# Kernel optimization log

Hardware: AMD Instinct MI355X
Metric: run time of the kernel (lower is better)

The kernel has to match this reference:

```python
import jax, jax.numpy as jnp
import numpy as np

B, L, D, H, S, V, K = 2, 64, 1024, 512, 50000, 40000, 32
SLM_LOGITS_SCALE = 0.1
BN_EPS = 1e-5


def setup_inputs() -> dict:
    key = jax.random.key(0)
    ks = jax.random.split(key, 8)
    return {
        "cached_embeddings": jax.random.normal(ks[0], (B, L, D), dtype=jnp.float32),
        "bn_gamma": jnp.ones((L,), jnp.float32),
        "bn_beta": jnp.zeros((L,), jnp.float32),
        "W1": jax.random.normal(ks[1], (D, H), dtype=jnp.float32) * 0.02,
        "b1": jnp.zeros((H,), jnp.float32),
        "W2": jax.random.normal(ks[2], (H, S), dtype=jnp.float32) * 0.02,
        "b2": jnp.zeros((S,), jnp.float32),
        "W_slm": jax.random.normal(ks[3], (H, V), dtype=jnp.float32) * 0.02,
        "b_slm": jnp.zeros((V,), jnp.float32),
        # fixed degree k=32 with values 1/min(deg,k) = 1/32 (full-degree rows)
        "sl_weights": jnp.full((S, K), 1.0 / K, jnp.float32),
        "sl_idx": jax.random.randint(ks[4], (S, K), 0, V, dtype=jnp.int32),
    }


def reference(cached_embeddings, bn_gamma, bn_beta, W1, b1, W2, b2,
              W_slm, b_slm, sl_weights, sl_idx):
    x = cached_embeddings  # [B, L, D]
    # BatchNorm1d(win_size): channels are sequence positions; stats over (B, D)
    mean = jnp.mean(x, axis=(0, 2), keepdims=True)
    var = jnp.var(x, axis=(0, 2), keepdims=True)
    xn = (x - mean) * jax.lax.rsqrt(var + BN_EPS)
    x = xn * bn_gamma[None, :, None] + bn_beta[None, :, None]
    # DenseEncoder: hidden + sense logits
    h = jax.nn.relu(jnp.einsum('bld,dh->blh', x, W1) + b1)  # [B, L, H]
    y = jnp.einsum('blh,hs->bls', h, W2) + b2                # [B, L, S]
    # SLM head: lemma logits
    v = jnp.einsum('blh,hv->blv', h, W_slm) + b_slm          # [B, L, V]
    # sparse sense->lemma matmul == weighted bounded-degree gather-sum
    g = v[..., sl_idx]                                       # [B, L, S, K]
    slm_logits = jnp.einsum('blsk,sk->bls', g, sl_weights)   # [B, L, S]
    return y + slm_logits * SLM_LOGITS_SCALE
```

## Files before the change

### kernel.cpp

```cpp
#include <hip/hip_runtime.h>

#define LL 64
#define DD 1024
#define HH 512
#define SS 50000
#define VV 40000
#define KD 32
#define MM 128

typedef __bf16 bf16_t;
typedef __bf16 bf16x8 __attribute__((ext_vector_type(8)));
typedef __bf16 bf16x4 __attribute__((ext_vector_type(4)));
typedef __bf16 bf16x2 __attribute__((ext_vector_type(2)));
typedef float f32x4 __attribute__((ext_vector_type(4)));

__device__ __forceinline__ void async_ld16(const void* g, void* l) {
    __builtin_amdgcn_global_load_lds(
        (const __attribute__((address_space(1))) void*)g,
        (__attribute__((address_space(3))) void*)l, 16, 0, 0);
}

__global__ __launch_bounds__(256) void k_bn(const float* __restrict__ x,
        const float* __restrict__ gamma, const float* __restrict__ beta,
        bf16_t* __restrict__ xn) {
    int l = blockIdx.x;
    int t = threadIdx.x;
    int b = t >> 7;
    int d0 = (t & 127) << 3;
    const float* xp = x + (size_t)(b * LL + l) * DD + d0;
    float4 v0 = *(const float4*)xp;
    float4 v1 = *(const float4*)(xp + 4);
    float s  = v0.x + v0.y + v0.z + v0.w + v1.x + v1.y + v1.z + v1.w;
    float ss = v0.x*v0.x + v0.y*v0.y + v0.z*v0.z + v0.w*v0.w
             + v1.x*v1.x + v1.y*v1.y + v1.z*v1.z + v1.w*v1.w;
    #pragma unroll
    for (int off = 32; off > 0; off >>= 1) {
        s  += __shfl_xor(s, off);
        ss += __shfl_xor(ss, off);
    }
    __shared__ float red[8];
    int wv = t >> 6, ln = t & 63;
    if (ln == 0) { red[wv] = s; red[4 + wv] = ss; }
    __syncthreads();
    float tot  = red[0] + red[1] + red[2] + red[3];
    float tots = red[4] + red[5] + red[6] + red[7];
    float mean = tot * (1.0f / 2048.0f);
    float var  = tots * (1.0f / 2048.0f) - mean * mean;
    float rstd = rsqrtf(var + 1e-5f);
    float g   = gamma[l] * rstd;
    float ofs = beta[l] - mean * g;
    bf16x8 o;
    o[0] = (bf16_t)(v0.x * g + ofs);
    o[1] = (bf16_t)(v0.y * g + ofs);
    o[2] = (bf16_t)(v0.z * g + ofs);
    o[3] = (bf16_t)(v0.w * g + ofs);
    o[4] = (bf16_t)(v1.x * g + ofs);
    o[5] = (bf16_t)(v1.y * g + ofs);
    o[6] = (bf16_t)(v1.z * g + ofs);
    o[7] = (bf16_t)(v1.w * g + ofs);
    *(bf16x8*)(xn + (size_t)(b * LL + l) * DD + d0) = o;
}

__global__ __launch_bounds__(256) void k_gemm1(const bf16_t* __restrict__ xn,
        const float* __restrict__ W1, const float* __restrict__ b1,
        bf16_t* __restrict__ h) {
    int t = threadIdx.x;
    int wv = t >> 6, lane = t & 63;
    int c = lane & 15, q = lane >> 4;
    int tile = blockIdx.x * 4 + wv;
    int tm = tile >> 5, tn = tile & 31;
    int col = tn * 16 + c;
    f32x4 acc = {};
    for (int kk = 0; kk < DD; kk += 32) {
        bf16x8 afr = *(const bf16x8*)(xn + (size_t)(tm * 16 + c) * DD + kk + q * 8);
        bf16x8 bfr;
        #pragma unroll
        for (int j = 0; j < 8; ++j)
            bfr[j] = (bf16_t)W1[(size_t)(kk + q * 8 + j) * HH + col];
        acc = __builtin_amdgcn_mfma_f32_16x16x32_bf16(afr, bfr, acc, 0, 0, 0);
    }
    float bias = b1[col];
    #pragma unroll
    for (int r = 0; r < 4; ++r) {
        int m = tm * 16 + q * 4 + r;
        float v = acc[r] + bias;
        h[(size_t)m * HH + col] = (bf16_t)(v > 0.f ? v : 0.f);
    }
}

__global__ __launch_bounds__(256) void k_gemm_v(const bf16_t* __restrict__ h,
        const float* __restrict__ Wslm, const float* __restrict__ bslm,
        bf16_t* __restrict__ vT) {
    __shared__ float wt[2][32 * 64];
    int t = threadIdx.x;
    int wv = t >> 6, lane = t & 63;
    int c = lane & 15, q = lane >> 4;
    int nb = blockIdx.x * 64;
    int col = nb + wv * 16 + c;
    int r  = t >> 4, sg = t & 15;
    const float* g0 = Wslm + (size_t)r        * VV + nb + sg * 4;
    const float* g1 = Wslm + (size_t)(r + 16) * VV + nb + sg * 4;

    #define STAGE_V(buf, kk) do { \
        async_ld16(g0 + (size_t)(kk) * VV, &wt[buf][t * 4]); \
        async_ld16(g1 + (size_t)(kk) * VV, &wt[buf][(t + 256) * 4]); } while (0)

    STAGE_V(0, 0);
    f32x4 acc[8] = {};
    #pragma unroll 1
    for (int step = 0; step < 16; ++step) {
        int cur = step & 1;
        __syncthreads();
        if (step < 15) STAGE_V(cur ^ 1, (step + 1) * 32);
        int kk = step * 32;
        bf16x8 bfr;
        #pragma unroll
        for (int j = 0; j < 8; ++j)
            bfr[j] = (bf16_t)wt[cur][(q * 8 + j) * 64 + wv * 16 + c];
        #pragma unroll
        for (int ms = 0; ms < 8; ++ms) {
            bf16x8 afr = *(const bf16x8*)(h + (size_t)(ms * 16 + c) * HH + kk + q * 8);
            acc[ms] = __builtin_amdgcn_mfma_f32_16x16x32_bf16(afr, bfr, acc[ms], 0, 0, 0);
        }
    }
    float bias = bslm[col];
    #pragma unroll
    for (int ms = 0; ms < 8; ++ms) {
        bf16x4 o;
        #pragma unroll
        for (int rr = 0; rr < 4; ++rr) o[rr] = (bf16_t)(acc[ms][rr] + bias);
        *(bf16x4*)(vT + (size_t)col * MM + ms * 16 + q * 4) = o;
    }
    #undef STAGE_V
}

__global__ __launch_bounds__(256) void k_gather(const bf16_t* __restrict__ vT,
        const float* __restrict__ slw, const int* __restrict__ slidx,
        bf16_t* __restrict__ slm) {
    int t = threadIdx.x;
    int wv = t >> 6, lane = t & 63;
    int s = blockIdx.x * 4 + wv;
    int idv = slidx[(size_t)s * KD + (lane & 31)];
    float wgt = slw[(size_t)s * KD + (lane & 31)];
    unsigned int u[KD];
    #pragma unroll
    for (int k = 0; k < KD; ++k) {
        int id = __shfl(idv, k);
        u[k] = *(const unsigned int*)(vT + (size_t)id * MM + lane * 2);
    }
    float a0 = 0.f, a1 = 0.f;
    #pragma unroll
    for (int k = 0; k < KD; ++k) {
        float w = __shfl(wgt, k);
        a0 += w * __uint_as_float(u[k] << 16);
        a1 += w * __uint_as_float(u[k] & 0xffff0000u);
    }
    bf16x2 o;
    o[0] = (bf16_t)a0;
    o[1] = (bf16_t)a1;
    *(bf16x2*)(slm + (size_t)s * MM + lane * 2) = o;
}

__global__ __launch_bounds__(256) void k_gemm_y(const bf16_t* __restrict__ h,
        const float* __restrict__ W2, const float* __restrict__ b2,
        const bf16_t* __restrict__ slm, float* __restrict__ out) {
    __shared__ float wt[2][32 * 64];
    int t = threadIdx.x;
    int wv = t >> 6, lane = t & 63;
    int c = lane & 15, q = lane >> 4;
    int nb = blockIdx.x * 64;
    int col = nb + wv * 16 + c;
    int r  = t >> 4, sg = t & 15;
    int sgc = nb + sg * 4;
    bool ok = (sgc + 4 <= SS);
    const float* g0 = ok ? (W2 + (size_t)r        * SS + sgc) : W2;
    const float* g1 = ok ? (W2 + (size_t)(r + 16) * SS + sgc) : W2;

    #define STAGE_Y(buf, kk) do { \
        async_ld16(g0 + (size_t)(kk) * SS, &wt[buf][t * 4]); \
        async_ld16(g1 + (size_t)(kk) * SS, &wt[buf][(t + 256) * 4]); } while (0)

    STAGE_Y(0, 0);
    f32x4 acc[8] = {};
    #pragma unroll 1
    for (int step = 0; step < 16; ++step) {
        int cur = step & 1;
        __syncthreads();
        if (step < 15) STAGE_Y(cur ^ 1, (step + 1) * 32);
        int kk = step * 32;
        bf16x8 bfr;
        #pragma unroll
        for (int j = 0; j < 8; ++j)
            bfr[j] = (bf16_t)wt[cur][(q * 8 + j) * 64 + wv * 16 + c];
        #pragma unroll
        for (int ms = 0; ms < 8; ++ms) {
            bf16x8 afr = *(const bf16x8*)(h + (size_t)(ms * 16 + c) * HH + kk + q * 8);
            acc[ms] = __builtin_amdgcn_mfma_f32_16x16x32_bf16(afr, bfr, acc[ms], 0, 0, 0);
        }
    }
    if (col < SS) {
        float bias = b2[col];
        #pragma unroll
        for (int ms = 0; ms < 8; ++ms) {
            bf16x4 sv = *(const bf16x4*)(slm + (size_t)col * MM + ms * 16 + q * 4);
            #pragma unroll
            for (int rr = 0; rr < 4; ++rr) {
                int m = ms * 16 + q * 4 + rr;
                out[(size_t)m * SS + col] = acc[ms][rr] + bias + 0.1f * (float)sv[rr];
            }
        }
    }
    #undef STAGE_Y
}

extern "C" void kernel_launch(void* const* d_in, const int* in_sizes, int n_in,
                              void* d_out, int out_size, void* d_ws, size_t ws_size,
                              hipStream_t stream) {
    const float* x     = (const float*)d_in[0];
    const float* gamma = (const float*)d_in[1];
    const float* beta  = (const float*)d_in[2];
    const float* W1    = (const float*)d_in[3];
    const float* b1    = (const float*)d_in[4];
    const float* W2    = (const float*)d_in[5];
    const float* b2    = (const float*)d_in[6];
    const float* Wslm  = (const float*)d_in[7];
    const float* bslm  = (const float*)d_in[8];
    const float* slw   = (const float*)d_in[9];
    const int*   slidx = (const int*)d_in[10];
    float* out = (float*)d_out;

    char* ws = (char*)d_ws;
    bf16_t* xn  = (bf16_t*)ws;
    bf16_t* h   = (bf16_t*)(ws + 262144);
    bf16_t* vT  = (bf16_t*)(ws + 393216);
    bf16_t* slm = (bf16_t*)(ws + 10633216);

    k_bn    <<<64,    256, 0, stream>>>(x, gamma, beta, xn);
    k_gemm1 <<<64,    256, 0, stream>>>(xn, W1, b1, h);
    k_gemm_v<<<625,   256, 0, stream>>>(h, Wslm, bslm, vT);
    k_gather<<<12500, 256, 0, stream>>>(vT, slw, slidx, slm);
    k_gemm_y<<<782,   256, 0, stream>>>(h, W2, b2, slm, out);
}
```

Before: 352.3 us.

## Store lemma logits as fp8, split-K gemm1, deeper staging with staggered K order

The lemma-logit intermediate vT is now stored as fp8 e4m3 instead of bf16, which halves the write traffic in k_gemm_v and the random-gather traffic in k_gather, at the cost of precision in the sense-lemma term. k_gemm1 now splits K across two waves per 16x16 tile and combines the partial sums through shared memory, giving 256 blocks instead of 64. The W_slm and W2 GEMMs stage 64 K-rows per step instead of 32, using 8 steps and twice the LDS. They also rotate each block's starting K offset by a per-block phase, likely to spread concurrent loads across memory channels.

```diff
diff --git a/kernel.cpp b/kernel.cpp
--- a/kernel.cpp
+++ b/kernel.cpp
@@ -1,4 +1,5 @@
 #include <hip/hip_runtime.h>
+#include <hip/hip_fp8.h>
 
 #define LL 64
 #define DD 1024
@@ -61,17 +62,17 @@
     *(bf16x8*)(xn + (size_t)(b * LL + l) * DD + d0) = o;
 }
 
-__global__ __launch_bounds__(256) void k_gemm1(const bf16_t* __restrict__ xn,
+__global__ __launch_bounds__(128) void k_gemm1(const bf16_t* __restrict__ xn,
         const float* __restrict__ W1, const float* __restrict__ b1,
         bf16_t* __restrict__ h) {
     int t = threadIdx.x;
     int wv = t >> 6, lane = t & 63;
     int c = lane & 15, q = lane >> 4;
-    int tile = blockIdx.x * 4 + wv;
+    int tile = blockIdx.x;
     int tm = tile >> 5, tn = tile & 31;
     int col = tn * 16 + c;
     f32x4 acc = {};
-    for (int kk = 0; kk < DD; kk += 32) {
+    for (int kk = wv * 512; kk < wv * 512 + 512; kk += 32) {
         bf16x8 afr = *(const bf16x8*)(xn + (size_t)(tm * 16 + c) * DD + kk + q * 8);
         bf16x8 bfr;
         #pragma unroll
@@ -79,62 +80,79 @@
             bfr[j] = (bf16_t)W1[(size_t)(kk + q * 8 + j) * HH + col];
         acc = __builtin_amdgcn_mfma_f32_16x16x32_bf16(afr, bfr, acc, 0, 0, 0);
     }
-    float bias = b1[col];
-    #pragma unroll
-    for (int r = 0; r < 4; ++r) {
-        int m = tm * 16 + q * 4 + r;
-        float v = acc[r] + bias;
-        h[(size_t)m * HH + col] = (bf16_t)(v > 0.f ? v : 0.f);
+    __shared__ float red[64 * 4];
+    if (wv == 1) {
+        #pragma unroll
+        for (int r = 0; r < 4; ++r) red[lane * 4 + r] = acc[r];
+    }
+    __syncthreads();
+    if (wv == 0) {
+        float bias = b1[col];
+        #pragma unroll
+        for (int r = 0; r < 4; ++r) {
+            int m = tm * 16 + q * 4 + r;
+            float v = acc[r] + red[lane * 4 + r] + bias;
+            h[(size_t)m * HH + col] = (bf16_t)(v > 0.f ? v : 0.f);
+        }
     }
 }
 
 __global__ __launch_bounds__(256) void k_gemm_v(const bf16_t* __restrict__ h,
         const float* __restrict__ Wslm, const float* __restrict__ bslm,
-        bf16_t* __restrict__ vT) {
-    __shared__ float wt[2][32 * 64];
+        unsigned char* __restrict__ vT8) {
+    __shared__ float wt[2][64 * 64];
     int t = threadIdx.x;
     int wv = t >> 6, lane = t & 63;
     int c = lane & 15, q = lane >> 4;
     int nb = blockIdx.x * 64;
     int col = nb + wv * 16 + c;
     int r  = t >> 4, sg = t & 15;
-    const float* g0 = Wslm + (size_t)r        * VV + nb + sg * 4;
-    const float* g1 = Wslm + (size_t)(r + 16) * VV + nb + sg * 4;
+    int phase = (blockIdx.x * 5) & 7;
+    const float* gbase = Wslm + (size_t)r * VV + nb + sg * 4;
 
     #define STAGE_V(buf, kk) do { \
-        async_ld16(g0 + (size_t)(kk) * VV, &wt[buf][t * 4]); \
-        async_ld16(g1 + (size_t)(kk) * VV, &wt[buf][(t + 256) * 4]); } while (0)
-
-    STAGE_V(0, 0);
+        _Pragma("unroll") \
+        for (int i = 0; i < 4; ++i) \
+            async_ld16(gbase + (size_t)((kk) + 16 * i) * VV, \
+                       &wt[buf][t * 4 + i * 1024]); } while (0)
+
+    STAGE_V(0, phase * 64);
     f32x4 acc[8] = {};
     #pragma unroll 1
-    for (int step = 0; step < 16; ++step) {
+    for (int step = 0; step < 8; ++step) {
         int cur = step & 1;
         __syncthreads();
-        if (step < 15) STAGE_V(cur ^ 1, (step + 1) * 32);
-        int kk = step * 32;
-        bf16x8 bfr;
-        #pragma unroll
-        for (int j = 0; j < 8; ++j)
-            bfr[j] = (bf16_t)wt[cur][(q * 8 + j) * 64 + wv * 16 + c];
-        #pragma unroll
-        for (int ms = 0; ms < 8; ++ms) {
-            bf16x8 afr = *(const bf16x8*)(h + (size_t)(ms * 16 + c) * HH + kk + q * 8);
-            acc[ms] = __builtin_amdgcn_mfma_f32_16x16x32_bf16(afr, bfr, acc[ms], 0, 0, 0);
+        if (step < 7) STAGE_V(cur ^ 1, (((step + 1 + phase) & 7) * 64));
+        int kk = ((step + phase) & 7) * 64;
+        #pragma unroll
+        for (int kh = 0; kh < 2; ++kh) {
+            bf16x8 bfr;
+            #pragma unroll
+            for (int j = 0; j < 8; ++j)
+                bfr[j] = (bf16_t)wt[cur][(kh * 32 + q * 8 + j) * 64 + wv * 16 + c];
+            #pragma unroll
+            for (int ms = 0; ms < 8; ++ms) {
+                bf16x8 afr = *(const bf16x8*)(h + (size_t)(ms * 16 + c) * HH
+                                              + kk + kh * 32 + q * 8);
+                acc[ms] = __builtin_amdgcn_mfma_f32_16x16x32_bf16(afr, bfr, acc[ms], 0, 0, 0);
+            }
         }
     }
     float bias = bslm[col];
     #pragma unroll
     for (int ms = 0; ms < 8; ++ms) {
-        bf16x4 o;
-        #pragma unroll
-        for (int rr = 0; rr < 4; ++rr) o[rr] = (bf16_t)(acc[ms][rr] + bias);
-        *(bf16x4*)(vT + (size_t)col * MM + ms * 16 + q * 4) = o;
+        union { unsigned int u; unsigned char b[4]; } pk;
+        #pragma unroll
+        for (int rr = 0; rr < 4; ++rr) {
+            __hip_fp8_e4m3 f8(acc[ms][rr] + bias);
+            pk.b[rr] = f8.__x;
+        }
+        *(unsigned int*)(vT8 + (size_t)col * MM + ms * 16 + q * 4) = pk.u;
     }
     #undef STAGE_V
 }
 
-__global__ __launch_bounds__(256) void k_gather(const bf16_t* __restrict__ vT,
+__global__ __launch_bounds__(256) void k_gather(const unsigned char* __restrict__ vT8,
         const float* __restrict__ slw, const int* __restrict__ slidx,
         bf16_t* __restrict__ slm) {
     int t = threadIdx.x;
@@ -142,18 +160,21 @@
     int s = blockIdx.x * 4 + wv;
     int idv = slidx[(size_t)s * KD + (lane & 31)];
     float wgt = slw[(size_t)s * KD + (lane & 31)];
-    unsigned int u[KD];
+    unsigned short u[KD];
     #pragma unroll
     for (int k = 0; k < KD; ++k) {
         int id = __shfl(idv, k);
-        u[k] = *(const unsigned int*)(vT + (size_t)id * MM + lane * 2);
+        u[k] = *(const unsigned short*)(vT8 + (size_t)id * MM + lane * 2);
     }
     float a0 = 0.f, a1 = 0.f;
     #pragma unroll
     for (int k = 0; k < KD; ++k) {
         float w = __shfl(wgt, k);
-        a0 += w * __uint_as_float(u[k] << 16);
-        a1 += w * __uint_as_float(u[k] & 0xffff0000u);
+        __hip_fp8_e4m3 f0, f1;
+        f0.__x = (unsigned char)(u[k] & 0xff);
+        f1.__x = (unsigned char)(u[k] >> 8);
+        a0 += w * (float)f0;
+        a1 += w * (float)f1;
     }
     bf16x2 o;
     o[0] = (bf16_t)a0;
@@ -164,7 +185,7 @@
 __global__ __launch_bounds__(256) void k_gemm_y(const bf16_t* __restrict__ h,
         const float* __restrict__ W2, const float* __restrict__ b2,
         const bf16_t* __restrict__ slm, float* __restrict__ out) {
-    __shared__ float wt[2][32 * 64];
+    __shared__ float wt[2][64 * 64];
     int t = threadIdx.x;
     int wv = t >> 6, lane = t & 63;
     int c = lane & 15, q = lane >> 4;
@@ -173,29 +194,35 @@
     int r  = t >> 4, sg = t & 15;
     int sgc = nb + sg * 4;
     bool ok = (sgc + 4 <= SS);
-    const float* g0 = ok ? (W2 + (size_t)r        * SS + sgc) : W2;
-    const float* g1 = ok ? (W2 + (size_t)(r + 16) * SS + sgc) : W2;
+    const float* gbase = ok ? (W2 + (size_t)r * SS + sgc) : W2;
+    int phase = (blockIdx.x * 5) & 7;
 
     #define STAGE_Y(buf, kk) do { \
-        async_ld16(g0 + (size_t)(kk) * SS, &wt[buf][t * 4]); \
-        async_ld16(g1 + (size_t)(kk) * SS, &wt[buf][(t + 256) * 4]); } while (0)
-
-    STAGE_Y(0, 0);
+        _Pragma("unroll") \
+        for (int i = 0; i < 4; ++i) \
+            async_ld16(gbase + (size_t)((kk) + 16 * i) * SS, \
+                       &wt[buf][t * 4 + i * 1024]); } while (0)
+
+    STAGE_Y(0, phase * 64);
     f32x4 acc[8] = {};
     #pragma unroll 1
-    for (int step = 0; step < 16; ++step) {
+    for (int step = 0; step < 8; ++step) {
         int cur = step & 1;
         __syncthreads();
-        if (step < 15) STAGE_Y(cur ^ 1, (step + 1) * 32);
-        int kk = step * 32;
-        bf16x8 bfr;
-        #pragma unroll
-        for (int j = 0; j < 8; ++j)
-            bfr[j] = (bf16_t)wt[cur][(q * 8 + j) * 64 + wv * 16 + c];
-        #pragma unroll
-        for (int ms = 0; ms < 8; ++ms) {
-            bf16x8 afr = *(const bf16x8*)(h + (size_t)(ms * 16 + c) * HH + kk + q * 8);
-            acc[ms] = __builtin_amdgcn_mfma_f32_16x16x32_bf16(afr, bfr, acc[ms], 0, 0, 0);
+        if (step < 7) STAGE_Y(cur ^ 1, (((step + 1 + phase) & 7) * 64));
+        int kk = ((step + phase) & 7) * 64;
+        #pragma unroll
+        for (int kh = 0; kh < 2; ++kh) {
+            bf16x8 bfr;
+            #pragma unroll
+            for (int j = 0; j < 8; ++j)
+                bfr[j] = (bf16_t)wt[cur][(kh * 32 + q * 8 + j) * 64 + wv * 16 + c];
+            #pragma unroll
+            for (int ms = 0; ms < 8; ++ms) {
+                bf16x8 afr = *(const bf16x8*)(h + (size_t)(ms * 16 + c) * HH
+                                              + kk + kh * 32 + q * 8);
+                acc[ms] = __builtin_amdgcn_mfma_f32_16x16x32_bf16(afr, bfr, acc[ms], 0, 0, 0);
+            }
         }
     }
     if (col < SS) {
@@ -230,14 +257,14 @@
     float* out = (float*)d_out;
 
     char* ws = (char*)d_ws;
-    bf16_t* xn  = (bf16_t*)ws;
-    bf16_t* h   = (bf16_t*)(ws + 262144);
-    bf16_t* vT  = (bf16_t*)(ws + 393216);
-    bf16_t* slm = (bf16_t*)(ws + 10633216);
+    bf16_t*        xn  = (bf16_t*)ws;
+    bf16_t*        h   = (bf16_t*)(ws + 262144);
+    unsigned char* vT8 = (unsigned char*)(ws + 393216);
+    bf16_t*        slm = (bf16_t*)(ws + 5513216);
 
     k_bn    <<<64,    256, 0, stream>>>(x, gamma, beta, xn);
-    k_gemm1 <<<64,    256, 0, stream>>>(xn, W1, b1, h);
-    k_gemm_v<<<625,   256, 0, stream>>>(h, Wslm, bslm, vT);
-    k_gather<<<12500, 256, 0, stream>>>(vT, slw, slidx, slm);
+    k_gemm1 <<<256,   128, 0, stream>>>(xn, W1, b1, h);
+    k_gemm_v<<<625,   256, 0, stream>>>(h, Wslm, bslm, vT8);
+    k_gather<<<12500, 256, 0, stream>>>(vT8, slw, slidx, slm);
     k_gemm_y<<<782,   256, 0, stream>>>(h, W2, b2, slm, out);
 }
```

Measured after the change: 364.9 us. 3.6% more time.
